# Optimization experiments

Hardware: AMD Instinct MI355X
Metric: run time of the kernel (lower is better)

Reference implementation:

```python
import jax, jax.numpy as jnp
import numpy as np

N_NODES = 50000


def setup_inputs() -> dict:
    key = jax.random.key(0)
    k1, k2, k3, k4 = jax.random.split(key, 4)
    x = jax.random.normal(k1, (N_NODES, 128), dtype=jnp.float32)
    edge_index = jax.random.randint(k2, (2, 1600000), 0, N_NODES, dtype=jnp.int64)
    W1 = jax.random.normal(k3, (128, 256), dtype=jnp.float32) * (1.0 / np.sqrt(128))
    b1 = jnp.zeros((256,), dtype=jnp.float32)
    W2 = jax.random.normal(k4, (256, 1), dtype=jnp.float32) * (1.0 / np.sqrt(256))
    b2 = jnp.zeros((1,), dtype=jnp.float32)
    return {"x": x, "edge_index": edge_index, "W1": W1, "b1": b1, "W2": W2, "b2": b2}


def _gcn_conv(x, src, dst, norm, W, b, n_nodes):
    # PyG GCNConv: h = X W; out_i = sum_j norm_ij * h_j (+ self loop) + b
    h = x @ W                               # [N, F_out]
    msg = h[src] * norm[:, None]            # [E', F_out] gather + scale
    out = jax.ops.segment_sum(msg, dst, num_segments=n_nodes)  # scatter-add
    return out + b


def reference(x, edge_index, W1, b1, W2, b2):
    n = x.shape[0]
    loop = jnp.arange(n, dtype=edge_index.dtype)
    src = jnp.concatenate([edge_index[0], loop])   # add self loops
    dst = jnp.concatenate([edge_index[1], loop])
    # symmetric degree normalization on A + I
    deg = jax.ops.segment_sum(jnp.ones_like(dst, dtype=x.dtype), dst, num_segments=n)
    dis = jnp.where(deg > 0, jax.lax.rsqrt(deg), 0.0)
    norm = dis[src] * dis[dst]                     # [E']
    h = jax.nn.relu(_gcn_conv(x, src, dst, norm, W1, b1, n))
    return _gcn_conv(h, src, dst, norm, W2, b2, n)
```

## Files before the change

### kernel.cpp

```cpp
#include <hip/hip_runtime.h>


#define EPB_LOG 12
#define EPB (1 << EPB_LOG)
#define BW_LOG 7
#define BW (1 << BW_LOG)
#define MAXBUCK 512
#define SCAN_TILE 2048
#define AMSTRIDE 136

typedef __attribute__((ext_vector_type(8))) short bf16x8;
typedef __attribute__((ext_vector_type(4))) float f32x4;

__device__ inline unsigned short f2bf(float f) {
    unsigned int b = __float_as_uint(f);
    unsigned int r = b + 0x7FFFu + ((b >> 16) & 1u);
    return (unsigned short)(r >> 16);
}
__device__ inline float bf_lo(unsigned int u) { return __uint_as_float(u << 16); }
__device__ inline float bf_hi(unsigned int u) { return __uint_as_float(u & 0xFFFF0000u); }

__device__ inline int detect_stride(const int* edges, int t, int* sh) {
    if (t < 64) {
        int v = edges[2 * t + 1];
        unsigned long long bb = __ballot(v != 0);
        if (t == 0) *sh = bb ? 1 : 2;
    }
    __syncthreads();
    return *sh;
}


__global__ __launch_bounds__(256) void k_count(
        const int* __restrict__ edges, const float* __restrict__ W1,
        unsigned short* __restrict__ w1t, int* __restrict__ btot_raw,
        long long E, int nbuck, int nsb) {
    int b = blockIdx.x, t = threadIdx.x;
    if (b >= nsb) {
        int row = (b - nsb) * 2 + (t >> 7);
        int k = t & 127;
        w1t[row * 128 + k] = f2bf(W1[k * 256 + row]);
        return;
    }
    __shared__ int bins[MAXBUCK];
    __shared__ int sh;
    for (int i = t; i < nbuck; i += 256) bins[i] = 0;
    int stride = detect_stride(edges, t, &sh);
    long long base = (long long)b << EPB_LOG;
    long long rem = E - base;
    int nE = (rem < (long long)EPB) ? (int)rem : EPB;
    for (int i = t; i < nE; i += 256) {
        int d = edges[(E + base + i) * stride];
        atomicAdd(&bins[d >> BW_LOG], 1);
    }
    __syncthreads();
    for (int i = t; i < nbuck; i += 256)
        if (bins[i]) atomicAdd(&btot_raw[i], bins[i]);
}

__global__ __launch_bounds__(256) void k_btot_scan(
        const int* __restrict__ btot_raw, int* __restrict__ btot,
        int* __restrict__ curg, int nbuck) {
    __shared__ int ws4[4];
    int t = threadIdx.x;
    int c4 = (nbuck + 255) >> 8;
    int lo = t * c4;
    int hi = lo + c4; if (hi > nbuck) hi = nbuck;
    if (lo > nbuck) lo = nbuck;
    int vals[2];
    int local = 0;
    for (int i = lo; i < hi; ++i) { vals[i - lo] = btot_raw[i]; local += vals[i - lo]; }
    int lane = t & 63, w = t >> 6;
    int inc = local;
    for (int off = 1; off < 64; off <<= 1) {
        int u = __shfl_up(inc, off, 64);
        if (lane >= off) inc += u;
    }
    if (lane == 63) ws4[w] = inc;
    __syncthreads();
    int woff = 0;
    for (int i = 0; i < w; ++i) woff += ws4[i];
    int ex = woff + inc - local;
    for (int i = lo; i < hi; ++i) {
        btot[i] = ex; curg[i] = ex;
        ex += vals[i - lo];
    }
}

__global__ __launch_bounds__(256) void k_partition(
        const int* __restrict__ edges, int* __restrict__ curg,
        unsigned int* __restrict__ part, long long E, int nbuck) {
    __shared__ unsigned int stage[EPB];
    __shared__ unsigned short dst16[EPB];
    __shared__ int bins[MAXBUCK];
    __shared__ int lcur[MAXBUCK];
    __shared__ int gbase[MAXBUCK];
    __shared__ int ws4[4];
    __shared__ int sh;
    int sb = blockIdx.x, t = threadIdx.x;
    for (int i = t; i < nbuck; i += 256) bins[i] = 0;
    int stride = detect_stride(edges, t, &sh);
    long long base = (long long)sb << EPB_LOG;
    long long rem = E - base;
    int nE = (rem < (long long)EPB) ? (int)rem : EPB;
    for (int i = t; i < nE; i += 256) {
        int d = edges[(E + base + i) * stride];
        dst16[i] = (unsigned short)d;
        atomicAdd(&bins[d >> BW_LOG], 1);
    }
    __syncthreads();
    int c4 = (nbuck + 255) >> 8;
    int lo = t * c4;
    int hi = lo + c4; if (hi > nbuck) hi = nbuck;
    if (lo > nbuck) lo = nbuck;
    int vals[2];
    int local = 0;
    for (int i = lo; i < hi; ++i) { vals[i - lo] = bins[i]; local += vals[i - lo]; }
    for (int i = t; i < nbuck; i += 256) {
        int c = bins[i];
        gbase[i] = c ? atomicAdd(&curg[i], c) : 0;
    }
    __syncthreads();
    int lane = t & 63, w = t >> 6;
    int inc = local;
    for (int off = 1; off < 64; off <<= 1) {
        int u = __shfl_up(inc, off, 64);
        if (lane >= off) inc += u;
    }
    if (lane == 63) ws4[w] = inc;
    __syncthreads();
    int woff = 0;
    for (int i = 0; i < w; ++i) woff += ws4[i];
    int ex = woff + inc - local;
    for (int i = lo; i < hi; ++i) {
        bins[i] = ex;
        lcur[i] = ex;
        ex += vals[i - lo];
    }
    __syncthreads();
    for (int i = t; i < nE; i += 256) {
        int s = edges[(base + i) * stride];
        int d = dst16[i];
        int b = d >> BW_LOG;
        int p = atomicAdd(&lcur[b], 1);
        stage[p] = ((unsigned int)s << 16) | (unsigned int)d;
    }
    __syncthreads();
    for (int i = t; i < nE; i += 256) {
        unsigned int pk = stage[i];
        int b = (int)(pk & 0xFFFFu) >> BW_LOG;
        part[gbase[b] + (i - bins[b])] = pk;
    }
}

__global__ __launch_bounds__(256) void k_build_csr(
        const unsigned int* __restrict__ part, const int* __restrict__ btot,
        const float* __restrict__ x, int* __restrict__ row_start,
        float* __restrict__ dis, int* __restrict__ csr_src,
        unsigned short* __restrict__ xs, int nbuck, int n, long long E) {
    __shared__ int c128[BW];
    __shared__ int lcur[BW];
    __shared__ float dld[BW];
    __shared__ int ws2[2];
    int b = blockIdx.x, t = threadIdx.x;
    if (t < BW) c128[t] = 0;
    __syncthreads();
    int start = btot[b];
    int endp = (b + 1 < nbuck) ? btot[b + 1] : (int)E;
    for (int i = start + t; i < endp; i += 256)
        atomicAdd(&c128[part[i] & (BW - 1)], 1);
    __syncthreads();
    int lane = t & 63, w = t >> 6;
    int deg = (t < BW) ? c128[t] : 0;
    int inc = deg;
    for (int off = 1; off < 64; off <<= 1) {
        int u = __shfl_up(inc, off, 64);
        if (lane >= off) inc += u;
    }
    if (t < BW && lane == 63) ws2[w] = inc;
    __syncthreads();
    if (t < BW) {
        int ex = inc - deg + ((w == 1) ? ws2[0] : 0);
        lcur[t] = ex;
        int d = (b << BW_LOG) + t;
        if (d < n) {
            row_start[d] = start + ex;
            float dv = rsqrtf((float)deg + 1.0f);
            dis[d] = dv;
            dld[t] = dv;
        }
    }
    if (b == nbuck - 1 && t == 0) row_start[n] = (int)E;
    __syncthreads();
    for (int i = start + t; i < endp; i += 256) {
        unsigned int pk = part[i];
        int r = atomicAdd(&lcur[pk & (BW - 1)], 1);
        csr_src[start + r] = (int)(pk >> 16);
    }
    int d0 = b << BW_LOG;
    for (int idx = t; idx < BW * 32; idx += 256) {
        int node = d0 + (idx >> 5);
        if (node >= n) break;
        float dv = dld[idx >> 5];
        float4 v = ((const float4*)x)[(size_t)node * 32 + (idx & 31)];
        ushort4 o;
        o.x = f2bf(v.x * dv); o.y = f2bf(v.y * dv);
        o.z = f2bf(v.z * dv); o.w = f2bf(v.w * dv);
        ((ushort4*)xs)[(size_t)node * 32 + (idx & 31)] = o;
    }
}

__global__ __launch_bounds__(512) void k_agg_mm(
        const unsigned short* __restrict__ xs, const int* __restrict__ csr_src,
        const int* __restrict__ rs, const float* __restrict__ dis,
        const unsigned short* __restrict__ w1t, const float* __restrict__ b1,
        const float* __restrict__ W2, float* __restrict__ svs, int n) {
    __shared__ short am[64 * AMSTRIDE];
    int t = threadIdx.x;
    int lane = t & 63, w = t >> 6;
    int blk = blockIdx.x;
    const unsigned int* xsu = (const unsigned int*)xs;
#pragma unroll 1
    for (int jj = 0; jj < 8; ++jj) {
        int r = w * 8 + jj;
        int node = blk * 64 + r;
        unsigned int pack = 0;
        if (node < n) {
            int start = rs[node], end = rs[node + 1];
            unsigned int self = xsu[((size_t)node << 6) + lane];
            float a0 = bf_lo(self), a1 = bf_hi(self);
            int e = start;
            for (; e + 7 < end; e += 8) {
                int s0 = csr_src[e],     s1 = csr_src[e + 1];
                int s2 = csr_src[e + 2], s3 = csr_src[e + 3];
                int s4 = csr_src[e + 4], s5 = csr_src[e + 5];
                int s6 = csr_src[e + 6], s7 = csr_src[e + 7];
                unsigned int v0 = xsu[((size_t)s0 << 6) + lane];
                unsigned int v1 = xsu[((size_t)s1 << 6) + lane];
                unsigned int v2 = xsu[((size_t)s2 << 6) + lane];
                unsigned int v3 = xsu[((size_t)s3 << 6) + lane];
                unsigned int v4 = xsu[((size_t)s4 << 6) + lane];
                unsigned int v5 = xsu[((size_t)s5 << 6) + lane];
                unsigned int v6 = xsu[((size_t)s6 << 6) + lane];
                unsigned int v7 = xsu[((size_t)s7 << 6) + lane];
                a0 += bf_lo(v0); a1 += bf_hi(v0);
                a0 += bf_lo(v1); a1 += bf_hi(v1);
                a0 += bf_lo(v2); a1 += bf_hi(v2);
                a0 += bf_lo(v3); a1 += bf_hi(v3);
                a0 += bf_lo(v4); a1 += bf_hi(v4);
                a0 += bf_lo(v5); a1 += bf_hi(v5);
                a0 += bf_lo(v6); a1 += bf_hi(v6);
                a0 += bf_lo(v7); a1 += bf_hi(v7);
            }
            for (; e < end; ++e) {
                int s0 = csr_src[e];
                unsigned int v0 = xsu[((size_t)s0 << 6) + lane];
                a0 += bf_lo(v0); a1 += bf_hi(v0);
            }
            float dn = dis[node];
            pack = (unsigned int)f2bf(a0 * dn) | ((unsigned int)f2bf(a1 * dn) << 16);
        }
        *(unsigned int*)&am[r * AMSTRIDE + 2 * lane] = pack;
    }
    __syncthreads();
    if (w >= 4) return;
    int m = lane & 15;
    int quad = lane >> 4;
    int node0 = blk * 64 + w * 16;

    bf16x8 afrag[4];
    const short* arow = &am[(w * 16 + m) * AMSTRIDE + quad * 8];
#pragma unroll
    for (int ks = 0; ks < 4; ++ks)
        afrag[ks] = *(const bf16x8*)(arow + ks * 32);

    float p0 = 0.f, p1 = 0.f, p2 = 0.f, p3 = 0.f;
#pragma unroll 1
    for (int tt = 0; tt < 16; ++tt) {
        const unsigned short* brow = w1t + (size_t)(tt * 16 + m) * 128 + quad * 8;
        f32x4 acc = {0.f, 0.f, 0.f, 0.f};
#pragma unroll
        for (int ks = 0; ks < 4; ++ks) {
            bf16x8 bfrag = *(const bf16x8*)(brow + ks * 32);
            acc = __builtin_amdgcn_mfma_f32_16x16x32_bf16(afrag[ks], bfrag, acc, 0, 0, 0);
        }
        int col = tt * 16 + m;
        float bb = b1[col], w2 = W2[col];
        float h0 = acc[0] + bb, h1 = acc[1] + bb, h2 = acc[2] + bb, h3 = acc[3] + bb;
        p0 += (h0 > 0.f ? h0 : 0.f) * w2;
        p1 += (h1 > 0.f ? h1 : 0.f) * w2;
        p2 += (h2 > 0.f ? h2 : 0.f) * w2;
        p3 += (h3 > 0.f ? h3 : 0.f) * w2;
    }
#pragma unroll
    for (int off = 1; off < 16; off <<= 1) {
        p0 += __shfl_xor(p0, off, 64);
        p1 += __shfl_xor(p1, off, 64);
        p2 += __shfl_xor(p2, off, 64);
        p3 += __shfl_xor(p3, off, 64);
    }
    if (m == 0) {
        int nb = node0 + quad * 4;
        if (nb + 0 < n) svs[nb + 0] = p0 * dis[nb + 0];
        if (nb + 1 < n) svs[nb + 1] = p1 * dis[nb + 1];
        if (nb + 2 < n) svs[nb + 2] = p2 * dis[nb + 2];
        if (nb + 3 < n) svs[nb + 3] = p3 * dis[nb + 3];
    }
}

__global__ __launch_bounds__(256) void k_out(
        const float* __restrict__ svs, const int* __restrict__ csr_src,
        const int* __restrict__ row_start, const float* __restrict__ dis,
        const float* __restrict__ b2, float* __restrict__ out, int n) {
    int wid  = (blockIdx.x * blockDim.x + threadIdx.x) >> 6;
    int lane = threadIdx.x & 63;
    if (wid >= n) return;
    int start = row_start[wid], end = row_start[wid + 1];
    float acc = 0.f;
    for (int e = start + lane; e < end; e += 64)
        acc += svs[csr_src[e]];
    for (int off = 32; off; off >>= 1) acc += __shfl_down(acc, off, 64);
    if (lane == 0)
        out[wid] = dis[wid] * (acc + svs[wid]) + b2[0];
}

__global__ void k_init(const int* __restrict__ edges, int* __restrict__ flag,
                       int* __restrict__ cnt, int n) {
    int i = blockIdx.x * blockDim.x + threadIdx.x;
    if (i < n) cnt[i] = 0;
    if (blockIdx.x == 0 && threadIdx.x < 64) {
        int v = edges[2 * threadIdx.x + 1];
        unsigned long long b = __ballot(v != 0);
        if (threadIdx.x == 0) flag[0] = b ? 1 : 2;
    }
}
__global__ __launch_bounds__(128) void k_prep_w(const float* __restrict__ W1,
        unsigned short* __restrict__ w1t) {
    int nn = blockIdx.x, k = threadIdx.x;
    w1t[nn * 128 + k] = f2bf(W1[k * 256 + nn]);
}
__global__ __launch_bounds__(256) void k_prep_xs(const float* __restrict__ x,
        const float* __restrict__ dis, unsigned short* __restrict__ xs, int n) {
    int i = blockIdx.x * 256 + threadIdx.x;
    if (i >= n * 32) return;
    float dsc = dis[i >> 5];
    float4 v = ((const float4*)x)[i];
    ushort4 o;
    o.x = f2bf(v.x * dsc); o.y = f2bf(v.y * dsc);
    o.z = f2bf(v.z * dsc); o.w = f2bf(v.w * dsc);
    ((ushort4*)xs)[i] = o;
}
__global__ void k_count_slow(const int* __restrict__ edges, const int* __restrict__ flag,
                             int* __restrict__ cnt, int* __restrict__ posi, long long E) {
    long long e = (long long)blockIdx.x * blockDim.x + threadIdx.x;
    if (e >= E) return;
    int stride = flag[0];
    int d = edges[(E + e) * stride];
    posi[e] = atomicAdd(&cnt[d], 1);
}
__global__ __launch_bounds__(256) void k_scan_partial(
        const int* __restrict__ cnt, int* __restrict__ bsum, int n) {
    int t = threadIdx.x;
    int idx = blockIdx.x * SCAN_TILE + t * 8;
    int s = 0;
#pragma unroll
    for (int j = 0; j < 8; ++j) { int i = idx + j; if (i < n) s += cnt[i]; }
    for (int off = 32; off; off >>= 1) s += __shfl_down(s, off, 64);
    __shared__ int ws[4];
    if ((t & 63) == 0) ws[t >> 6] = s;
    __syncthreads();
    if (t == 0) bsum[blockIdx.x] = ws[0] + ws[1] + ws[2] + ws[3];
}
__global__ void k_scan_tops(int* __restrict__ bsum, int nb) {
    int t = threadIdx.x;
    int w = (t < nb) ? bsum[t] : 0;
    int v = w;
    for (int off = 1; off < 64; off <<= 1) {
        int u = __shfl_up(v, off, 64);
        if (t >= off) v += u;
    }
    if (t < nb) bsum[t] = v - w;
}
__global__ __launch_bounds__(256) void k_scan_apply(
        const int* __restrict__ cnt, const int* __restrict__ bsum,
        int* __restrict__ row_start, float* __restrict__ dis, int n) {
    int t = threadIdx.x;
    int lane = t & 63, w = t >> 6;
    int idx = blockIdx.x * SCAN_TILE + t * 8;
    int vals[8];
    int s = 0;
#pragma unroll
    for (int j = 0; j < 8; ++j) { int i = idx + j; vals[j] = (i < n) ? cnt[i] : 0; s += vals[j]; }
    int inc = s;
    for (int off = 1; off < 64; off <<= 1) {
        int u = __shfl_up(inc, off, 64);
        if (lane >= off) inc += u;
    }
    __shared__ int wsum[4];
    if (lane == 63) wsum[w] = inc;
    __syncthreads();
    int woff = 0;
    for (int i = 0; i < w; ++i) woff += wsum[i];
    int ex = bsum[blockIdx.x] + woff + inc - s;
#pragma unroll
    for (int j = 0; j < 8; ++j) {
        int i = idx + j;
        if (i < n) {
            row_start[i] = ex;
            dis[i] = rsqrtf((float)vals[j] + 1.0f);
            ex += vals[j];
        }
    }
    if (idx <= n && n < idx + 8) row_start[n] = ex;
}
__global__ void k_scatter_slow(const int* __restrict__ edges, const int* __restrict__ flag,
                               const int* __restrict__ row_start, const int* __restrict__ posi,
                               int* __restrict__ csr_src, long long E) {
    long long e = (long long)blockIdx.x * blockDim.x + threadIdx.x;
    if (e >= E) return;
    int stride = flag[0];
    int s = edges[e * stride];
    int d = edges[(E + e) * stride];
    csr_src[row_start[d] + posi[e]] = s;
}
__global__ __launch_bounds__(256) void k_agg(
        const unsigned short* __restrict__ xs, const int* __restrict__ csr_src,
        const int* __restrict__ row_start, const float* __restrict__ dis,
        unsigned short* __restrict__ aggh, int n) {
    int wid  = (blockIdx.x * blockDim.x + threadIdx.x) >> 6;
    int lane = threadIdx.x & 63;
    if (wid >= n) return;
    int start = row_start[wid], end = row_start[wid + 1];
    unsigned int self = ((const unsigned int*)xs)[((size_t)wid << 6) + lane];
    float a0 = bf_lo(self), a1 = bf_hi(self);
    for (int e = start; e < end; ++e) {
        int s0 = csr_src[e];
        unsigned int v0 = ((const unsigned int*)xs)[((size_t)s0 << 6) + lane];
        a0 += bf_lo(v0); a1 += bf_hi(v0);
    }
    float dn = dis[wid];
    unsigned int pack = (unsigned int)f2bf(a0 * dn) | ((unsigned int)f2bf(a1 * dn) << 16);
    ((unsigned int*)aggh)[((size_t)wid << 6) + lane] = pack;
}
__global__ __launch_bounds__(256) void k_mm(
        const unsigned short* __restrict__ aggh, const unsigned short* __restrict__ w1t,
        const float* __restrict__ b1, const float* __restrict__ W2,
        const float* __restrict__ dis, float* __restrict__ svs, int n) {
    int wave = threadIdx.x >> 6;
    int lane = threadIdx.x & 63;
    int m = lane & 15, quad = lane >> 4;
    int node0 = blockIdx.x * 64 + wave * 16;
    bf16x8 afrag[4];
    const unsigned short* arow = aggh + (size_t)(node0 + m) * 128 + quad * 8;
#pragma unroll
    for (int ks = 0; ks < 4; ++ks) afrag[ks] = *(const bf16x8*)(arow + ks * 32);
    float p0 = 0.f, p1 = 0.f, p2 = 0.f, p3 = 0.f;
#pragma unroll 1
    for (int tt = 0; tt < 16; ++tt) {
        const unsigned short* brow = w1t + (size_t)(tt * 16 + m) * 128 + quad * 8;
        f32x4 acc = {0.f, 0.f, 0.f, 0.f};
#pragma unroll
        for (int ks = 0; ks < 4; ++ks) {
            bf16x8 bfrag = *(const bf16x8*)(brow + ks * 32);
            acc = __builtin_amdgcn_mfma_f32_16x16x32_bf16(afrag[ks], bfrag, acc, 0, 0, 0);
        }
        int col = tt * 16 + m;
        float bb = b1[col], w2 = W2[col];
        float h0 = acc[0] + bb, h1 = acc[1] + bb, h2 = acc[2] + bb, h3 = acc[3] + bb;
        p0 += (h0 > 0.f ? h0 : 0.f) * w2;
        p1 += (h1 > 0.f ? h1 : 0.f) * w2;
        p2 += (h2 > 0.f ? h2 : 0.f) * w2;
        p3 += (h3 > 0.f ? h3 : 0.f) * w2;
    }
#pragma unroll
    for (int off = 1; off < 16; off <<= 1) {
        p0 += __shfl_xor(p0, off, 64);
        p1 += __shfl_xor(p1, off, 64);
        p2 += __shfl_xor(p2, off, 64);
        p3 += __shfl_xor(p3, off, 64);
    }
    if (m == 0) {
        int nb = node0 + quad * 4;
        if (nb + 0 < n) svs[nb + 0] = p0 * dis[nb + 0];
        if (nb + 1 < n) svs[nb + 1] = p1 * dis[nb + 1];
        if (nb + 2 < n) svs[nb + 2] = p2 * dis[nb + 2];
        if (nb + 3 < n) svs[nb + 3] = p3 * dis[nb + 3];
    }
}

extern "C" void kernel_launch(void* const* d_in, const int* in_sizes, int n_in,
                              void* d_out, int out_size, void* d_ws, size_t ws_size,
                              hipStream_t stream) {
    const float* x  = (const float*)d_in[0];
    const int*   ei = (const int*)d_in[1];
    const float* W1 = (const float*)d_in[2];
    const float* b1 = (const float*)d_in[3];
    const float* W2 = (const float*)d_in[4];
    const float* b2 = (const float*)d_in[5];
    float* out = (float*)d_out;

    const int N = in_sizes[0] / 128;
    const long long E = in_sizes[1] / 2;
    const int nsb = (int)((E + EPB - 1) >> EPB_LOG);
    const int nbuck = (N + BW - 1) >> BW_LOG;

    char* ws = (char*)d_ws;
    size_t off = 0;
    auto take = [&](size_t bytes) -> char* {
        char* p = ws + off;
        off = (off + bytes + 255) & ~(size_t)255;
        return p;
    };
    int*            flag     = (int*)take(4);
    int*            cnt      = (int*)take((size_t)N * 4);
    int*            rs       = (int*)take((size_t)(N + 1) * 4);
    float*          dis      = (float*)take((size_t)N * 4);
    float*          svs      = (float*)take((size_t)N * 4);
    int*            bsum     = (int*)take(64 * 4);
    int*            btot_raw = (int*)take(MAXBUCK * 4);
    int*            btot     = (int*)take(MAXBUCK * 4);
    int*            curg     = (int*)take(MAXBUCK * 4);
    unsigned int*   part     = (unsigned int*)take((size_t)E * 4);
    int*            csr_src  = (int*)take((size_t)E * 4);
    unsigned short* xs       = (unsigned short*)take((size_t)N * 128 * 2);
    unsigned short* w1t      = (unsigned short*)take((size_t)256 * 128 * 2);
    unsigned short* aggh     = (unsigned short*)take((size_t)(N + 64) * 128 * 2);

    int nb_n  = (N + 255) / 256;
    int nb_e  = (int)((E + 255) / 256);
    int nb_s  = (N + SCAN_TILE - 1) / SCAN_TILE;
    int nb_x  = (N * 32 + 255) / 256;
    int nb_am = (N + 63) / 64;

    bool fast = (N < 65536);

    if (fast) {
        hipMemsetAsync(btot_raw, 0, (size_t)nbuck * 4, stream);
        k_count    <<<nsb + 128, 256, 0, stream>>>(ei, W1, w1t, btot_raw, E, nbuck, nsb);
        k_btot_scan<<<1, 256, 0, stream>>>(btot_raw, btot, curg, nbuck);
        k_partition<<<nsb, 256, 0, stream>>>(ei, curg, part, E, nbuck);
        k_build_csr<<<nbuck, 256, 0, stream>>>(part, btot, x, rs, dis, csr_src,
                                               xs, nbuck, N, E);
        k_agg_mm   <<<nb_am, 512, 0, stream>>>(xs, csr_src, rs, dis, w1t, b1, W2, svs, N);
        k_out      <<<(N + 3) / 4, 256, 0, stream>>>(svs, csr_src, rs, dis, b2, out, N);
    } else {
        k_init        <<<nb_n, 256, 0, stream>>>(ei, flag, cnt, N);
        k_prep_w      <<<256, 128, 0, stream>>>(W1, w1t);
        k_count_slow  <<<nb_e, 256, 0, stream>>>(ei, flag, cnt, (int*)part, E);
        k_scan_partial<<<nb_s, 256, 0, stream>>>(cnt, bsum, N);
        k_scan_tops   <<<1, 64, 0, stream>>>(bsum, nb_s);
        k_scan_apply  <<<nb_s, 256, 0, stream>>>(cnt, bsum, rs, dis, N);
        k_prep_xs     <<<nb_x, 256, 0, stream>>>(x, dis, xs, N);
        k_scatter_slow<<<nb_e, 256, 0, stream>>>(ei, flag, rs, (const int*)part, csr_src, E);
        k_agg         <<<(N + 3) / 4, 256, 0, stream>>>(xs, csr_src, rs, dis, aggh, N);
        k_mm          <<<(N + 63) / 64, 256, 0, stream>>>(aggh, w1t, b1, W2, dis, svs, N);
        k_out         <<<(N + 3) / 4, 256, 0, stream>>>(svs, csr_src, rs, dis, b2, out, N);
    }
}
```

Baseline: 237.8 us.

## Fuse GCN pipeline into single persistent cooperative kernel with grid syncs

Replaces the multi-kernel fast path (count, scan, partition, CSR build, aggregate+matmul, output) with one persistent cooperative kernel that loops over work items per stage and separates stages with grid-wide syncs. The goal is to remove per-launch overhead and the idle tails between the many small kernels. In exchange, the aggregation and matmul stages are split again through a global bf16 buffer instead of shared memory. The grid is limited to occupancy-resident blocks, and the large shared staging array may cap occupancy, with the old launches kept as fallback if the cooperative launch fails.

```diff
diff --git a/kernel.cpp b/kernel.cpp
--- a/kernel.cpp
+++ b/kernel.cpp
@@ -1,4 +1,7 @@
 #include <hip/hip_runtime.h>
+#include <hip/hip_cooperative_groups.h>
+
+namespace cg = cooperative_groups;
 
 
 #define EPB_LOG 12
@@ -7,7 +10,6 @@
 #define BW (1 << BW_LOG)
 #define MAXBUCK 512
 #define SCAN_TILE 2048
-#define AMSTRIDE 136
 
 typedef __attribute__((ext_vector_type(8))) short bf16x8;
 typedef __attribute__((ext_vector_type(4))) float f32x4;
@@ -31,201 +33,188 @@
 }
 
 
-__global__ __launch_bounds__(256) void k_count(
-        const int* __restrict__ edges, const float* __restrict__ W1,
-        unsigned short* __restrict__ w1t, int* __restrict__ btot_raw,
-        long long E, int nbuck, int nsb) {
-    int b = blockIdx.x, t = threadIdx.x;
-    if (b >= nsb) {
-        int row = (b - nsb) * 2 + (t >> 7);
-        int k = t & 127;
-        w1t[row * 128 + k] = f2bf(W1[k * 256 + row]);
-        return;
-    }
-    __shared__ int bins[MAXBUCK];
-    __shared__ int sh;
-    for (int i = t; i < nbuck; i += 256) bins[i] = 0;
-    int stride = detect_stride(edges, t, &sh);
-    long long base = (long long)b << EPB_LOG;
-    long long rem = E - base;
-    int nE = (rem < (long long)EPB) ? (int)rem : EPB;
-    for (int i = t; i < nE; i += 256) {
-        int d = edges[(E + base + i) * stride];
-        atomicAdd(&bins[d >> BW_LOG], 1);
-    }
-    __syncthreads();
-    for (int i = t; i < nbuck; i += 256)
-        if (bins[i]) atomicAdd(&btot_raw[i], bins[i]);
-}
-
-__global__ __launch_bounds__(256) void k_btot_scan(
-        const int* __restrict__ btot_raw, int* __restrict__ btot,
-        int* __restrict__ curg, int nbuck) {
-    __shared__ int ws4[4];
-    int t = threadIdx.x;
-    int c4 = (nbuck + 255) >> 8;
-    int lo = t * c4;
-    int hi = lo + c4; if (hi > nbuck) hi = nbuck;
-    if (lo > nbuck) lo = nbuck;
-    int vals[2];
-    int local = 0;
-    for (int i = lo; i < hi; ++i) { vals[i - lo] = btot_raw[i]; local += vals[i - lo]; }
-    int lane = t & 63, w = t >> 6;
-    int inc = local;
-    for (int off = 1; off < 64; off <<= 1) {
-        int u = __shfl_up(inc, off, 64);
-        if (lane >= off) inc += u;
-    }
-    if (lane == 63) ws4[w] = inc;
-    __syncthreads();
-    int woff = 0;
-    for (int i = 0; i < w; ++i) woff += ws4[i];
-    int ex = woff + inc - local;
-    for (int i = lo; i < hi; ++i) {
-        btot[i] = ex; curg[i] = ex;
-        ex += vals[i - lo];
-    }
-}
-
-__global__ __launch_bounds__(256) void k_partition(
-        const int* __restrict__ edges, int* __restrict__ curg,
-        unsigned int* __restrict__ part, long long E, int nbuck) {
+__global__ __launch_bounds__(256) void k_all(
+        const int* __restrict__ edges, const float* __restrict__ x,
+        const float* __restrict__ W1, const float* __restrict__ b1,
+        const float* __restrict__ W2, const float* __restrict__ b2,
+        float* __restrict__ out, unsigned short* __restrict__ w1t,
+        int* __restrict__ btot_raw, int* __restrict__ btot,
+        int* __restrict__ curg, unsigned int* __restrict__ part,
+        int* __restrict__ csr_src, unsigned short* __restrict__ xs,
+        int* __restrict__ rs, float* __restrict__ dis,
+        float* __restrict__ svs, unsigned short* __restrict__ aggh,
+        int n, long long E, int nsb, int nbuck) {
+    cg::grid_group grid = cg::this_grid();
     __shared__ unsigned int stage[EPB];
-    __shared__ unsigned short dst16[EPB];
     __shared__ int bins[MAXBUCK];
     __shared__ int lcur[MAXBUCK];
     __shared__ int gbase[MAXBUCK];
     __shared__ int ws4[4];
     __shared__ int sh;
-    int sb = blockIdx.x, t = threadIdx.x;
-    for (int i = t; i < nbuck; i += 256) bins[i] = 0;
+    int t = threadIdx.x;
+    int B = blockIdx.x, NB = gridDim.x;
+    int lane = t & 63, w = t >> 6;
     int stride = detect_stride(edges, t, &sh);
-    long long base = (long long)sb << EPB_LOG;
-    long long rem = E - base;
-    int nE = (rem < (long long)EPB) ? (int)rem : EPB;
-    for (int i = t; i < nE; i += 256) {
-        int d = edges[(E + base + i) * stride];
-        dst16[i] = (unsigned short)d;
-        atomicAdd(&bins[d >> BW_LOG], 1);
-    }
-    __syncthreads();
-    int c4 = (nbuck + 255) >> 8;
-    int lo = t * c4;
-    int hi = lo + c4; if (hi > nbuck) hi = nbuck;
-    if (lo > nbuck) lo = nbuck;
-    int vals[2];
-    int local = 0;
-    for (int i = lo; i < hi; ++i) { vals[i - lo] = bins[i]; local += vals[i - lo]; }
-    for (int i = t; i < nbuck; i += 256) {
-        int c = bins[i];
-        gbase[i] = c ? atomicAdd(&curg[i], c) : 0;
-    }
-    __syncthreads();
-    int lane = t & 63, w = t >> 6;
-    int inc = local;
-    for (int off = 1; off < 64; off <<= 1) {
-        int u = __shfl_up(inc, off, 64);
-        if (lane >= off) inc += u;
-    }
-    if (lane == 63) ws4[w] = inc;
-    __syncthreads();
-    int woff = 0;
-    for (int i = 0; i < w; ++i) woff += ws4[i];
-    int ex = woff + inc - local;
-    for (int i = lo; i < hi; ++i) {
-        bins[i] = ex;
-        lcur[i] = ex;
-        ex += vals[i - lo];
-    }
-    __syncthreads();
-    for (int i = t; i < nE; i += 256) {
-        int s = edges[(base + i) * stride];
-        int d = dst16[i];
-        int b = d >> BW_LOG;
-        int p = atomicAdd(&lcur[b], 1);
-        stage[p] = ((unsigned int)s << 16) | (unsigned int)d;
-    }
-    __syncthreads();
-    for (int i = t; i < nE; i += 256) {
-        unsigned int pk = stage[i];
-        int b = (int)(pk & 0xFFFFu) >> BW_LOG;
-        part[gbase[b] + (i - bins[b])] = pk;
-    }
-}
-
-__global__ __launch_bounds__(256) void k_build_csr(
-        const unsigned int* __restrict__ part, const int* __restrict__ btot,
-        const float* __restrict__ x, int* __restrict__ row_start,
-        float* __restrict__ dis, int* __restrict__ csr_src,
-        unsigned short* __restrict__ xs, int nbuck, int n, long long E) {
-    __shared__ int c128[BW];
-    __shared__ int lcur[BW];
-    __shared__ float dld[BW];
-    __shared__ int ws2[2];
-    int b = blockIdx.x, t = threadIdx.x;
-    if (t < BW) c128[t] = 0;
-    __syncthreads();
-    int start = btot[b];
-    int endp = (b + 1 < nbuck) ? btot[b + 1] : (int)E;
-    for (int i = start + t; i < endp; i += 256)
-        atomicAdd(&c128[part[i] & (BW - 1)], 1);
-    __syncthreads();
-    int lane = t & 63, w = t >> 6;
-    int deg = (t < BW) ? c128[t] : 0;
-    int inc = deg;
-    for (int off = 1; off < 64; off <<= 1) {
-        int u = __shfl_up(inc, off, 64);
-        if (lane >= off) inc += u;
-    }
-    if (t < BW && lane == 63) ws2[w] = inc;
-    __syncthreads();
-    if (t < BW) {
-        int ex = inc - deg + ((w == 1) ? ws2[0] : 0);
-        lcur[t] = ex;
-        int d = (b << BW_LOG) + t;
-        if (d < n) {
-            row_start[d] = start + ex;
-            float dv = rsqrtf((float)deg + 1.0f);
-            dis[d] = dv;
-            dld[t] = dv;
-        }
-    }
-    if (b == nbuck - 1 && t == 0) row_start[n] = (int)E;
-    __syncthreads();
-    for (int i = start + t; i < endp; i += 256) {
-        unsigned int pk = part[i];
-        int r = atomicAdd(&lcur[pk & (BW - 1)], 1);
-        csr_src[start + r] = (int)(pk >> 16);
-    }
-    int d0 = b << BW_LOG;
-    for (int idx = t; idx < BW * 32; idx += 256) {
-        int node = d0 + (idx >> 5);
-        if (node >= n) break;
-        float dv = dld[idx >> 5];
-        float4 v = ((const float4*)x)[(size_t)node * 32 + (idx & 31)];
-        ushort4 o;
-        o.x = f2bf(v.x * dv); o.y = f2bf(v.y * dv);
-        o.z = f2bf(v.z * dv); o.w = f2bf(v.w * dv);
-        ((ushort4*)xs)[(size_t)node * 32 + (idx & 31)] = o;
-    }
-}
-
-__global__ __launch_bounds__(512) void k_agg_mm(
-        const unsigned short* __restrict__ xs, const int* __restrict__ csr_src,
-        const int* __restrict__ rs, const float* __restrict__ dis,
-        const unsigned short* __restrict__ w1t, const float* __restrict__ b1,
-        const float* __restrict__ W2, float* __restrict__ svs, int n) {
-    __shared__ short am[64 * AMSTRIDE];
-    int t = threadIdx.x;
-    int lane = t & 63, w = t >> 6;
-    int blk = blockIdx.x;
-    const unsigned int* xsu = (const unsigned int*)xs;
-#pragma unroll 1
-    for (int jj = 0; jj < 8; ++jj) {
-        int r = w * 8 + jj;
-        int node = blk * 64 + r;
-        unsigned int pack = 0;
-        if (node < n) {
+
+    for (int i = B * 256 + t; i < nbuck; i += NB * 256) btot_raw[i] = 0;
+    for (int i = B * 256 + t; i < 256 * 128; i += NB * 256) {
+        int row = i >> 7, k = i & 127;
+        w1t[i] = f2bf(W1[k * 256 + row]);
+    }
+    grid.sync();
+
+    for (int sb = B; sb < nsb; sb += NB) {
+        for (int i = t; i < nbuck; i += 256) bins[i] = 0;
+        __syncthreads();
+        long long base = (long long)sb << EPB_LOG;
+        long long rem = E - base;
+        int nE = (rem < (long long)EPB) ? (int)rem : EPB;
+        for (int i = t; i < nE; i += 256) {
+            int d = edges[(E + base + i) * stride];
+            atomicAdd(&bins[d >> BW_LOG], 1);
+        }
+        __syncthreads();
+        for (int i = t; i < nbuck; i += 256)
+            if (bins[i]) atomicAdd(&btot_raw[i], bins[i]);
+        __syncthreads();
+    }
+    grid.sync();
+
+    if (B == 0) {
+        int c4 = (nbuck + 255) >> 8;
+        int lo = t * c4;
+        int hi = lo + c4; if (hi > nbuck) hi = nbuck;
+        if (lo > nbuck) lo = nbuck;
+        int vals[2];
+        int local = 0;
+        for (int i = lo; i < hi; ++i) { vals[i - lo] = btot_raw[i]; local += vals[i - lo]; }
+        int inc = local;
+        for (int off = 1; off < 64; off <<= 1) {
+            int u = __shfl_up(inc, off, 64);
+            if (lane >= off) inc += u;
+        }
+        if (lane == 63) ws4[w] = inc;
+        __syncthreads();
+        int woff = 0;
+        for (int i = 0; i < w; ++i) woff += ws4[i];
+        int ex = woff + inc - local;
+        for (int i = lo; i < hi; ++i) {
+            btot[i] = ex; curg[i] = ex;
+            ex += vals[i - lo];
+        }
+    }
+    grid.sync();
+
+    for (int sb = B; sb < nsb; sb += NB) {
+        for (int i = t; i < nbuck; i += 256) bins[i] = 0;
+        __syncthreads();
+        long long base = (long long)sb << EPB_LOG;
+        long long rem = E - base;
+        int nE = (rem < (long long)EPB) ? (int)rem : EPB;
+        for (int i = t; i < nE; i += 256) {
+            int d = edges[(E + base + i) * stride];
+            atomicAdd(&bins[d >> BW_LOG], 1);
+        }
+        __syncthreads();
+        int c4 = (nbuck + 255) >> 8;
+        int lo = t * c4;
+        int hi = lo + c4; if (hi > nbuck) hi = nbuck;
+        if (lo > nbuck) lo = nbuck;
+        int vals[2];
+        int local = 0;
+        for (int i = lo; i < hi; ++i) { vals[i - lo] = bins[i]; local += vals[i - lo]; }
+        for (int i = t; i < nbuck; i += 256) {
+            int c = bins[i];
+            gbase[i] = c ? atomicAdd(&curg[i], c) : 0;
+        }
+        __syncthreads();
+        int inc = local;
+        for (int off = 1; off < 64; off <<= 1) {
+            int u = __shfl_up(inc, off, 64);
+            if (lane >= off) inc += u;
+        }
+        if (lane == 63) ws4[w] = inc;
+        __syncthreads();
+        int woff = 0;
+        for (int i = 0; i < w; ++i) woff += ws4[i];
+        int ex = woff + inc - local;
+        for (int i = lo; i < hi; ++i) {
+            bins[i] = ex;
+            lcur[i] = ex;
+            ex += vals[i - lo];
+        }
+        __syncthreads();
+        for (int i = t; i < nE; i += 256) {
+            int s = edges[(base + i) * stride];
+            int d = edges[(E + base + i) * stride];
+            int bk = d >> BW_LOG;
+            int p = atomicAdd(&lcur[bk], 1);
+            stage[p] = ((unsigned int)s << 16) | (unsigned int)d;
+        }
+        __syncthreads();
+        for (int i = t; i < nE; i += 256) {
+            unsigned int pk = stage[i];
+            int bk = (int)(pk & 0xFFFFu) >> BW_LOG;
+            part[gbase[bk] + (i - bins[bk])] = pk;
+        }
+        __syncthreads();
+    }
+    grid.sync();
+
+    if (B == 0 && t == 0) rs[n] = (int)E;
+    for (int b = B; b < nbuck; b += NB) {
+        int* c128 = bins;
+        float* dld = (float*)gbase;
+        if (t < BW) c128[t] = 0;
+        __syncthreads();
+        int start = btot[b];
+        int endp = (b + 1 < nbuck) ? btot[b + 1] : (int)E;
+        for (int i = start + t; i < endp; i += 256)
+            atomicAdd(&c128[part[i] & (BW - 1)], 1);
+        __syncthreads();
+        int deg = (t < BW) ? c128[t] : 0;
+        int inc = deg;
+        for (int off = 1; off < 64; off <<= 1) {
+            int u = __shfl_up(inc, off, 64);
+            if (lane >= off) inc += u;
+        }
+        if (t < BW && lane == 63) ws4[w] = inc;
+        __syncthreads();
+        if (t < BW) {
+            int ex = inc - deg + ((w == 1) ? ws4[0] : 0);
+            lcur[t] = ex;
+            int d = (b << BW_LOG) + t;
+            if (d < n) {
+                rs[d] = start + ex;
+                float dv = rsqrtf((float)deg + 1.0f);
+                dis[d] = dv;
+                dld[t] = dv;
+            }
+        }
+        __syncthreads();
+        for (int i = start + t; i < endp; i += 256) {
+            unsigned int pk = part[i];
+            int r = atomicAdd(&lcur[pk & (BW - 1)], 1);
+            csr_src[start + r] = (int)(pk >> 16);
+        }
+        int d0 = b << BW_LOG;
+        for (int idx = t; idx < BW * 32; idx += 256) {
+            int node = d0 + (idx >> 5);
+            if (node >= n) break;
+            float dv = dld[idx >> 5];
+            float4 v = ((const float4*)x)[(size_t)node * 32 + (idx & 31)];
+            ushort4 o;
+            o.x = f2bf(v.x * dv); o.y = f2bf(v.y * dv);
+            o.z = f2bf(v.z * dv); o.w = f2bf(v.w * dv);
+            ((ushort4*)xs)[(size_t)node * 32 + (idx & 31)] = o;
+        }
+        __syncthreads();
+    }
+    grid.sync();
+
+    {
+        const unsigned int* xsu = (const unsigned int*)xs;
+        for (int node = B * 4 + w; node < n; node += NB * 4) {
             int start = rs[node], end = rs[node + 1];
             unsigned int self = xsu[((size_t)node << 6) + lane];
             float a0 = bf_lo(self), a1 = bf_hi(self);
@@ -258,22 +247,304 @@
                 a0 += bf_lo(v0); a1 += bf_hi(v0);
             }
             float dn = dis[node];
-            pack = (unsigned int)f2bf(a0 * dn) | ((unsigned int)f2bf(a1 * dn) << 16);
-        }
-        *(unsigned int*)&am[r * AMSTRIDE + 2 * lane] = pack;
-    }
-    __syncthreads();
-    if (w >= 4) return;
-    int m = lane & 15;
-    int quad = lane >> 4;
-    int node0 = blk * 64 + w * 16;
-
+            unsigned int pack = (unsigned int)f2bf(a0 * dn)
+                              | ((unsigned int)f2bf(a1 * dn) << 16);
+            ((unsigned int*)aggh)[((size_t)node << 6) + lane] = pack;
+        }
+    }
+    grid.sync();
+
+    {
+        int m = lane & 15, quad = lane >> 4;
+        int ng = (n + 63) >> 6;
+        for (int g = B; g < ng; g += NB) {
+            int node0 = g * 64 + w * 16;
+            bf16x8 afrag[4];
+            const unsigned short* arow = aggh + (size_t)(node0 + m) * 128 + quad * 8;
+#pragma unroll
+            for (int ks = 0; ks < 4; ++ks)
+                afrag[ks] = *(const bf16x8*)(arow + ks * 32);
+            float p0 = 0.f, p1 = 0.f, p2 = 0.f, p3 = 0.f;
+#pragma unroll 1
+            for (int tt = 0; tt < 16; ++tt) {
+                const unsigned short* brow = w1t + (size_t)(tt * 16 + m) * 128 + quad * 8;
+                f32x4 acc = {0.f, 0.f, 0.f, 0.f};
+#pragma unroll
+                for (int ks = 0; ks < 4; ++ks) {
+                    bf16x8 bfrag = *(const bf16x8*)(brow + ks * 32);
+                    acc = __builtin_amdgcn_mfma_f32_16x16x32_bf16(afrag[ks], bfrag, acc, 0, 0, 0);
+                }
+                int col = tt * 16 + m;
+                float bb = b1[col], w2 = W2[col];
+                float h0 = acc[0] + bb, h1 = acc[1] + bb, h2 = acc[2] + bb, h3 = acc[3] + bb;
+                p0 += (h0 > 0.f ? h0 : 0.f) * w2;
+                p1 += (h1 > 0.f ? h1 : 0.f) * w2;
+                p2 += (h2 > 0.f ? h2 : 0.f) * w2;
+                p3 += (h3 > 0.f ? h3 : 0.f) * w2;
+            }
+#pragma unroll
+            for (int off = 1; off < 16; off <<= 1) {
+                p0 += __shfl_xor(p0, off, 64);
+                p1 += __shfl_xor(p1, off, 64);
+                p2 += __shfl_xor(p2, off, 64);
+                p3 += __shfl_xor(p3, off, 64);
+            }
+            if (m == 0) {
+                int nb = node0 + quad * 4;
+                if (nb + 0 < n) svs[nb + 0] = p0 * dis[nb + 0];
+                if (nb + 1 < n) svs[nb + 1] = p1 * dis[nb + 1];
+                if (nb + 2 < n) svs[nb + 2] = p2 * dis[nb + 2];
+                if (nb + 3 < n) svs[nb + 3] = p3 * dis[nb + 3];
+            }
+        }
+    }
+    grid.sync();
+
+    for (int node = B * 4 + w; node < n; node += NB * 4) {
+        int start = rs[node], end = rs[node + 1];
+        float acc = 0.f;
+        for (int e = start + lane; e < end; e += 64)
+            acc += svs[csr_src[e]];
+        for (int off = 32; off; off >>= 1) acc += __shfl_down(acc, off, 64);
+        if (lane == 0)
+            out[node] = dis[node] * (acc + svs[node]) + b2[0];
+    }
+}
+
+
+__global__ __launch_bounds__(256) void k_count(
+        const int* __restrict__ edges, const float* __restrict__ W1,
+        unsigned short* __restrict__ w1t, int* __restrict__ btot_raw,
+        long long E, int nbuck, int nsb) {
+    int b = blockIdx.x, t = threadIdx.x;
+    if (b >= nsb) {
+        int row = (b - nsb) * 2 + (t >> 7);
+        int k = t & 127;
+        w1t[row * 128 + k] = f2bf(W1[k * 256 + row]);
+        return;
+    }
+    __shared__ int bins[MAXBUCK];
+    __shared__ int sh;
+    for (int i = t; i < nbuck; i += 256) bins[i] = 0;
+    int stride = detect_stride(edges, t, &sh);
+    long long base = (long long)b << EPB_LOG;
+    long long rem = E - base;
+    int nE = (rem < (long long)EPB) ? (int)rem : EPB;
+    for (int i = t; i < nE; i += 256) {
+        int d = edges[(E + base + i) * stride];
+        atomicAdd(&bins[d >> BW_LOG], 1);
+    }
+    __syncthreads();
+    for (int i = t; i < nbuck; i += 256)
+        if (bins[i]) atomicAdd(&btot_raw[i], bins[i]);
+}
+
+__global__ __launch_bounds__(256) void k_btot_scan(
+        const int* __restrict__ btot_raw, int* __restrict__ btot,
+        int* __restrict__ curg, int nbuck) {
+    __shared__ int ws4[4];
+    int t = threadIdx.x;
+    int c4 = (nbuck + 255) >> 8;
+    int lo = t * c4;
+    int hi = lo + c4; if (hi > nbuck) hi = nbuck;
+    if (lo > nbuck) lo = nbuck;
+    int vals[2];
+    int local = 0;
+    for (int i = lo; i < hi; ++i) { vals[i - lo] = btot_raw[i]; local += vals[i - lo]; }
+    int lane = t & 63, w = t >> 6;
+    int inc = local;
+    for (int off = 1; off < 64; off <<= 1) {
+        int u = __shfl_up(inc, off, 64);
+        if (lane >= off) inc += u;
+    }
+    if (lane == 63) ws4[w] = inc;
+    __syncthreads();
+    int woff = 0;
+    for (int i = 0; i < w; ++i) woff += ws4[i];
+    int ex = woff + inc - local;
+    for (int i = lo; i < hi; ++i) {
+        btot[i] = ex; curg[i] = ex;
+        ex += vals[i - lo];
+    }
+}
+
+__global__ __launch_bounds__(256) void k_partition(
+        const int* __restrict__ edges, int* __restrict__ curg,
+        unsigned int* __restrict__ part, long long E, int nbuck) {
+    __shared__ unsigned int stage[EPB];
+    __shared__ int bins[MAXBUCK];
+    __shared__ int lcur[MAXBUCK];
+    __shared__ int gbase[MAXBUCK];
+    __shared__ int ws4[4];
+    __shared__ int sh;
+    int sb = blockIdx.x, t = threadIdx.x;
+    for (int i = t; i < nbuck; i += 256) bins[i] = 0;
+    int stride = detect_stride(edges, t, &sh);
+    long long base = (long long)sb << EPB_LOG;
+    long long rem = E - base;
+    int nE = (rem < (long long)EPB) ? (int)rem : EPB;
+    for (int i = t; i < nE; i += 256) {
+        int d = edges[(E + base + i) * stride];
+        atomicAdd(&bins[d >> BW_LOG], 1);
+    }
+    __syncthreads();
+    int c4 = (nbuck + 255) >> 8;
+    int lo = t * c4;
+    int hi = lo + c4; if (hi > nbuck) hi = nbuck;
+    if (lo > nbuck) lo = nbuck;
+    int vals[2];
+    int local = 0;
+    for (int i = lo; i < hi; ++i) { vals[i - lo] = bins[i]; local += vals[i - lo]; }
+    for (int i = t; i < nbuck; i += 256) {
+        int c = bins[i];
+        gbase[i] = c ? atomicAdd(&curg[i], c) : 0;
+    }
+    __syncthreads();
+    int lane = t & 63, w = t >> 6;
+    int inc = local;
+    for (int off = 1; off < 64; off <<= 1) {
+        int u = __shfl_up(inc, off, 64);
+        if (lane >= off) inc += u;
+    }
+    if (lane == 63) ws4[w] = inc;
+    __syncthreads();
+    int woff = 0;
+    for (int i = 0; i < w; ++i) woff += ws4[i];
+    int ex = woff + inc - local;
+    for (int i = lo; i < hi; ++i) {
+        bins[i] = ex;
+        lcur[i] = ex;
+        ex += vals[i - lo];
+    }
+    __syncthreads();
+    for (int i = t; i < nE; i += 256) {
+        int s = edges[(base + i) * stride];
+        int d = edges[(E + base + i) * stride];
+        int bk = d >> BW_LOG;
+        int p = atomicAdd(&lcur[bk], 1);
+        stage[p] = ((unsigned int)s << 16) | (unsigned int)d;
+    }
+    __syncthreads();
+    for (int i = t; i < nE; i += 256) {
+        unsigned int pk = stage[i];
+        int bk = (int)(pk & 0xFFFFu) >> BW_LOG;
+        part[gbase[bk] + (i - bins[bk])] = pk;
+    }
+}
+
+__global__ __launch_bounds__(256) void k_build_csr(
+        const unsigned int* __restrict__ part, const int* __restrict__ btot,
+        const float* __restrict__ x, int* __restrict__ row_start,
+        float* __restrict__ dis, int* __restrict__ csr_src,
+        unsigned short* __restrict__ xs, int nbuck, int n, long long E) {
+    __shared__ int c128[BW];
+    __shared__ int lcur[BW];
+    __shared__ float dld[BW];
+    __shared__ int ws2[2];
+    int b = blockIdx.x, t = threadIdx.x;
+    if (t < BW) c128[t] = 0;
+    __syncthreads();
+    int start = btot[b];
+    int endp = (b + 1 < nbuck) ? btot[b + 1] : (int)E;
+    for (int i = start + t; i < endp; i += 256)
+        atomicAdd(&c128[part[i] & (BW - 1)], 1);
+    __syncthreads();
+    int lane = t & 63, w = t >> 6;
+    int deg = (t < BW) ? c128[t] : 0;
+    int inc = deg;
+    for (int off = 1; off < 64; off <<= 1) {
+        int u = __shfl_up(inc, off, 64);
+        if (lane >= off) inc += u;
+    }
+    if (t < BW && lane == 63) ws2[w] = inc;
+    __syncthreads();
+    if (t < BW) {
+        int ex = inc - deg + ((w == 1) ? ws2[0] : 0);
+        lcur[t] = ex;
+        int d = (b << BW_LOG) + t;
+        if (d < n) {
+            row_start[d] = start + ex;
+            float dv = rsqrtf((float)deg + 1.0f);
+            dis[d] = dv;
+            dld[t] = dv;
+        }
+    }
+    if (b == nbuck - 1 && t == 0) row_start[n] = (int)E;
+    __syncthreads();
+    for (int i = start + t; i < endp; i += 256) {
+        unsigned int pk = part[i];
+        int r = atomicAdd(&lcur[pk & (BW - 1)], 1);
+        csr_src[start + r] = (int)(pk >> 16);
+    }
+    int d0 = b << BW_LOG;
+    for (int idx = t; idx < BW * 32; idx += 256) {
+        int node = d0 + (idx >> 5);
+        if (node >= n) break;
+        float dv = dld[idx >> 5];
+        float4 v = ((const float4*)x)[(size_t)node * 32 + (idx & 31)];
+        ushort4 o;
+        o.x = f2bf(v.x * dv); o.y = f2bf(v.y * dv);
+        o.z = f2bf(v.z * dv); o.w = f2bf(v.w * dv);
+        ((ushort4*)xs)[(size_t)node * 32 + (idx & 31)] = o;
+    }
+}
+
+__global__ __launch_bounds__(256) void k_agg(
+        const unsigned short* __restrict__ xs, const int* __restrict__ csr_src,
+        const int* __restrict__ row_start, const float* __restrict__ dis,
+        unsigned short* __restrict__ aggh, int n) {
+    int wid  = (blockIdx.x * blockDim.x + threadIdx.x) >> 6;
+    int lane = threadIdx.x & 63;
+    if (wid >= n) return;
+    int start = row_start[wid], end = row_start[wid + 1];
+    const unsigned int* xsu = (const unsigned int*)xs;
+    unsigned int self = xsu[((size_t)wid << 6) + lane];
+    float a0 = bf_lo(self), a1 = bf_hi(self);
+    int e = start;
+    for (; e + 7 < end; e += 8) {
+        int s0 = csr_src[e],     s1 = csr_src[e + 1];
+        int s2 = csr_src[e + 2], s3 = csr_src[e + 3];
+        int s4 = csr_src[e + 4], s5 = csr_src[e + 5];
+        int s6 = csr_src[e + 6], s7 = csr_src[e + 7];
+        unsigned int v0 = xsu[((size_t)s0 << 6) + lane];
+        unsigned int v1 = xsu[((size_t)s1 << 6) + lane];
+        unsigned int v2 = xsu[((size_t)s2 << 6) + lane];
+        unsigned int v3 = xsu[((size_t)s3 << 6) + lane];
+        unsigned int v4 = xsu[((size_t)s4 << 6) + lane];
+        unsigned int v5 = xsu[((size_t)s5 << 6) + lane];
+        unsigned int v6 = xsu[((size_t)s6 << 6) + lane];
+        unsigned int v7 = xsu[((size_t)s7 << 6) + lane];
+        a0 += bf_lo(v0); a1 += bf_hi(v0);
+        a0 += bf_lo(v1); a1 += bf_hi(v1);
+        a0 += bf_lo(v2); a1 += bf_hi(v2);
+        a0 += bf_lo(v3); a1 += bf_hi(v3);
+        a0 += bf_lo(v4); a1 += bf_hi(v4);
+        a0 += bf_lo(v5); a1 += bf_hi(v5);
+        a0 += bf_lo(v6); a1 += bf_hi(v6);
+        a0 += bf_lo(v7); a1 += bf_hi(v7);
+    }
+    for (; e < end; ++e) {
+        int s0 = csr_src[e];
+        unsigned int v0 = xsu[((size_t)s0 << 6) + lane];
+        a0 += bf_lo(v0); a1 += bf_hi(v0);
+    }
+    float dn = dis[wid];
+    unsigned int pack = (unsigned int)f2bf(a0 * dn) | ((unsigned int)f2bf(a1 * dn) << 16);
+    ((unsigned int*)aggh)[((size_t)wid << 6) + lane] = pack;
+}
+
+__global__ __launch_bounds__(256) void k_mm(
+        const unsigned short* __restrict__ aggh, const unsigned short* __restrict__ w1t,
+        const float* __restrict__ b1, const float* __restrict__ W2,
+        const float* __restrict__ dis, float* __restrict__ svs, int n) {
+    int wave = threadIdx.x >> 6;
+    int lane = threadIdx.x & 63;
+    int m = lane & 15, quad = lane >> 4;
+    int node0 = blockIdx.x * 64 + wave * 16;
     bf16x8 afrag[4];
-    const short* arow = &am[(w * 16 + m) * AMSTRIDE + quad * 8];
-#pragma unroll
-    for (int ks = 0; ks < 4; ++ks)
-        afrag[ks] = *(const bf16x8*)(arow + ks * 32);
-
+    const unsigned short* arow = aggh + (size_t)(node0 + m) * 128 + quad * 8;
+#pragma unroll
+    for (int ks = 0; ks < 4; ++ks) afrag[ks] = *(const bf16x8*)(arow + ks * 32);
     float p0 = 0.f, p1 = 0.f, p2 = 0.f, p3 = 0.f;
 #pragma unroll 1
     for (int tt = 0; tt < 16; ++tt) {
@@ -334,11 +605,6 @@
         if (threadIdx.x == 0) flag[0] = b ? 1 : 2;
     }
 }
-__global__ __launch_bounds__(128) void k_prep_w(const float* __restrict__ W1,
-        unsigned short* __restrict__ w1t) {
-    int nn = blockIdx.x, k = threadIdx.x;
-    w1t[nn * 128 + k] = f2bf(W1[k * 256 + nn]);
-}
 __global__ __launch_bounds__(256) void k_prep_xs(const float* __restrict__ x,
         const float* __restrict__ dis, unsigned short* __restrict__ xs, int n) {
     int i = blockIdx.x * 256 + threadIdx.x;
@@ -350,6 +616,11 @@
     o.z = f2bf(v.z * dsc); o.w = f2bf(v.w * dsc);
     ((ushort4*)xs)[i] = o;
 }
+__global__ __launch_bounds__(128) void k_prep_w(const float* __restrict__ W1,
+        unsigned short* __restrict__ w1t) {
+    int nn = blockIdx.x, k = threadIdx.x;
+    w1t[nn * 128 + k] = f2bf(W1[k * 256 + nn]);
+}
 __global__ void k_count_slow(const int* __restrict__ edges, const int* __restrict__ flag,
                              int* __restrict__ cnt, int* __restrict__ posi, long long E) {
     long long e = (long long)blockIdx.x * blockDim.x + threadIdx.x;
@@ -422,70 +693,6 @@
     int s = edges[e * stride];
     int d = edges[(E + e) * stride];
     csr_src[row_start[d] + posi[e]] = s;
-}
-__global__ __launch_bounds__(256) void k_agg(
-        const unsigned short* __restrict__ xs, const int* __restrict__ csr_src,
-        const int* __restrict__ row_start, const float* __restrict__ dis,
-        unsigned short* __restrict__ aggh, int n) {
-    int wid  = (blockIdx.x * blockDim.x + threadIdx.x) >> 6;
-    int lane = threadIdx.x & 63;
-    if (wid >= n) return;
-    int start = row_start[wid], end = row_start[wid + 1];
-    unsigned int self = ((const unsigned int*)xs)[((size_t)wid << 6) + lane];
-    float a0 = bf_lo(self), a1 = bf_hi(self);
-    for (int e = start; e < end; ++e) {
-        int s0 = csr_src[e];
-        unsigned int v0 = ((const unsigned int*)xs)[((size_t)s0 << 6) + lane];
-        a0 += bf_lo(v0); a1 += bf_hi(v0);
-    }
-    float dn = dis[wid];
-    unsigned int pack = (unsigned int)f2bf(a0 * dn) | ((unsigned int)f2bf(a1 * dn) << 16);
-    ((unsigned int*)aggh)[((size_t)wid << 6) + lane] = pack;
-}
-__global__ __launch_bounds__(256) void k_mm(
-        const unsigned short* __restrict__ aggh, const unsigned short* __restrict__ w1t,
-        const float* __restrict__ b1, const float* __restrict__ W2,
-        const float* __restrict__ dis, float* __restrict__ svs, int n) {
-    int wave = threadIdx.x >> 6;
-    int lane = threadIdx.x & 63;
-    int m = lane & 15, quad = lane >> 4;
-    int node0 = blockIdx.x * 64 + wave * 16;
-    bf16x8 afrag[4];
-    const unsigned short* arow = aggh + (size_t)(node0 + m) * 128 + quad * 8;
-#pragma unroll
-    for (int ks = 0; ks < 4; ++ks) afrag[ks] = *(const bf16x8*)(arow + ks * 32);
-    float p0 = 0.f, p1 = 0.f, p2 = 0.f, p3 = 0.f;
-#pragma unroll 1
-    for (int tt = 0; tt < 16; ++tt) {
-        const unsigned short* brow = w1t + (size_t)(tt * 16 + m) * 128 + quad * 8;
-        f32x4 acc = {0.f, 0.f, 0.f, 0.f};
-#pragma unroll
-        for (int ks = 0; ks < 4; ++ks) {
-            bf16x8 bfrag = *(const bf16x8*)(brow + ks * 32);
-            acc = __builtin_amdgcn_mfma_f32_16x16x32_bf16(afrag[ks], bfrag, acc, 0, 0, 0);
-        }
-        int col = tt * 16 + m;
-        float bb = b1[col], w2 = W2[col];
-        float h0 = acc[0] + bb, h1 = acc[1] + bb, h2 = acc[2] + bb, h3 = acc[3] + bb;
-        p0 += (h0 > 0.f ? h0 : 0.f) * w2;
-        p1 += (h1 > 0.f ? h1 : 0.f) * w2;
-        p2 += (h2 > 0.f ? h2 : 0.f) * w2;
-        p3 += (h3 > 0.f ? h3 : 0.f) * w2;
-    }
-#pragma unroll
-    for (int off = 1; off < 16; off <<= 1) {
-        p0 += __shfl_xor(p0, off, 64);
-        p1 += __shfl_xor(p1, off, 64);
-        p2 += __shfl_xor(p2, off, 64);
-        p3 += __shfl_xor(p3, off, 64);
-    }
-    if (m == 0) {
-        int nb = node0 + quad * 4;
-        if (nb + 0 < n) svs[nb + 0] = p0 * dis[nb + 0];
-        if (nb + 1 < n) svs[nb + 1] = p1 * dis[nb + 1];
-        if (nb + 2 < n) svs[nb + 2] = p2 * dis[nb + 2];
-        if (nb + 3 < n) svs[nb + 3] = p3 * dis[nb + 3];
-    }
 }
 
 extern "C" void kernel_launch(void* const* d_in, const int* in_sizes, int n_in,
@@ -530,20 +737,44 @@
     int nb_e  = (int)((E + 255) / 256);
     int nb_s  = (N + SCAN_TILE - 1) / SCAN_TILE;
     int nb_x  = (N * 32 + 255) / 256;
-    int nb_am = (N + 63) / 64;
 
     bool fast = (N < 65536);
 
+    bool coop_done = false;
     if (fast) {
+        int dev = 0;
+        (void)hipGetDevice(&dev);
+        int numCU = 0;
+        (void)hipDeviceGetAttribute(&numCU, hipDeviceAttributeMultiprocessorCount, dev);
+        int perCU = 0;
+        (void)hipOccupancyMaxActiveBlocksPerMultiprocessor(&perCU, k_all, 256, 0);
+        long long nbL = (long long)perCU * (numCU > 0 ? numCU : 0);
+        int NB = (int)(nbL > 2048 ? 2048 : nbL);
+        if (NB > 0) {
+            int n_ = N; long long E_ = E; int nsb_ = nsb; int nbuck_ = nbuck;
+            void* args[] = { (void*)&ei, (void*)&x, (void*)&W1, (void*)&b1,
+                             (void*)&W2, (void*)&b2, (void*)&out, (void*)&w1t,
+                             (void*)&btot_raw, (void*)&btot, (void*)&curg,
+                             (void*)&part, (void*)&csr_src, (void*)&xs,
+                             (void*)&rs, (void*)&dis, (void*)&svs, (void*)&aggh,
+                             (void*)&n_, (void*)&E_, (void*)&nsb_, (void*)&nbuck_ };
+            hipError_t err = hipLaunchCooperativeKernel((void*)k_all, dim3(NB),
+                                                        dim3(256), args, 0, stream);
+            coop_done = (err == hipSuccess);
+        }
+    }
+
+    if (fast && !coop_done) {
         hipMemsetAsync(btot_raw, 0, (size_t)nbuck * 4, stream);
         k_count    <<<nsb + 128, 256, 0, stream>>>(ei, W1, w1t, btot_raw, E, nbuck, nsb);
         k_btot_scan<<<1, 256, 0, stream>>>(btot_raw, btot, curg, nbuck);
         k_partition<<<nsb, 256, 0, stream>>>(ei, curg, part, E, nbuck);
         k_build_csr<<<nbuck, 256, 0, stream>>>(part, btot, x, rs, dis, csr_src,
                                                xs, nbuck, N, E);
-        k_agg_mm   <<<nb_am, 512, 0, stream>>>(xs, csr_src, rs, dis, w1t, b1, W2, svs, N);
+        k_agg      <<<(N + 3) / 4, 256, 0, stream>>>(xs, csr_src, rs, dis, aggh, N);
+        k_mm       <<<(N + 63) / 64, 256, 0, stream>>>(aggh, w1t, b1, W2, dis, svs, N);
         k_out      <<<(N + 3) / 4, 256, 0, stream>>>(svs, csr_src, rs, dis, b2, out, N);
-    } else {
+    } else if (!fast) {
         k_init        <<<nb_n, 256, 0, stream>>>(ei, flag, cnt, N);
         k_prep_w      <<<256, 128, 0, stream>>>(W1, w1t);
         k_count_slow  <<<nb_e, 256, 0, stream>>>(ei, flag, cnt, (int*)part, E);
```

Result: slower. 827.3 us (+247.8%).
